# Kernel tuning notes

Hardware: AMD Instinct MI355X
Metric: run time of the kernel (lower is better)

The kernel has to match this reference:

```python
import jax, jax.numpy as jnp
import numpy as np

N, D, NH, NC, B, NL = 400, 256, 4, 2, 64, 2
HD = D // NH


def _ln(x, g, b, eps=1e-5):
    mu = x.mean(-1, keepdims=True)
    var = ((x - mu) ** 2).mean(-1, keepdims=True)
    return (x - mu) * jax.lax.rsqrt(var + eps) * g + b


def _mha(q, kv, wqkv, bqkv, wo, bo):
    # torch nn.MultiheadAttention (batch_first), eval mode
    wq, wk, wv = jnp.split(wqkv, 3, axis=0)
    bq, bk, bv = jnp.split(bqkv, 3, axis=0)
    Bsz, Sq, _ = q.shape
    Sk = kv.shape[1]
    qh = (q @ wq.T + bq).reshape(Bsz, Sq, NH, HD).transpose(0, 2, 1, 3)
    kh = (kv @ wk.T + bk).reshape(Bsz, Sk, NH, HD).transpose(0, 2, 1, 3)
    vh = (kv @ wv.T + bv).reshape(Bsz, Sk, NH, HD).transpose(0, 2, 1, 3)
    scores = jnp.einsum('bhqd,bhkd->bhqk', qh, kh) / jnp.sqrt(jnp.float32(HD))
    attn = jax.nn.softmax(scores, axis=-1)
    o = jnp.einsum('bhqk,bhkd->bhqd', attn, vh)
    o = o.transpose(0, 2, 1, 3).reshape(Bsz, Sq, D)
    return o @ wo.T + bo


def setup_inputs() -> dict:
    key = jax.random.key(0)
    ks = iter(jax.random.split(key, 64))
    w = lambda *s: (jax.random.normal(next(ks), s, dtype=jnp.float32) * 0.02)
    inp = {
        'fc_matrix': jax.random.uniform(next(ks), (B, N, N), dtype=jnp.float32),
        'sc_matrix': jax.random.uniform(next(ks), (B, N, N), dtype=jnp.float32),
        'proj_w': w(D, N), 'proj_b': jnp.zeros((D,), jnp.float32),
        'enc_qkv_w': w(NL, 3 * D, D), 'enc_qkv_b': jnp.zeros((NL, 3 * D), jnp.float32),
        'enc_out_w': w(NL, D, D), 'enc_out_b': jnp.zeros((NL, D), jnp.float32),
        'enc_lin1_w': w(NL, 4 * D, D), 'enc_lin1_b': jnp.zeros((NL, 4 * D), jnp.float32),
        'enc_lin2_w': w(NL, D, 4 * D), 'enc_lin2_b': jnp.zeros((NL, D), jnp.float32),
        'enc_n1_g': jnp.ones((NL, D), jnp.float32), 'enc_n1_b': jnp.zeros((NL, D), jnp.float32),
        'enc_n2_g': jnp.ones((NL, D), jnp.float32), 'enc_n2_b': jnp.zeros((NL, D), jnp.float32),
        'gcn_w1': w(D, N), 'gcn_b1': jnp.zeros((D,), jnp.float32),
        'gcn_w2': w(D, D), 'gcn_b2': jnp.zeros((D,), jnp.float32),
        'ca1_qkv_w': w(3 * D, D), 'ca1_qkv_b': jnp.zeros((3 * D,), jnp.float32),
        'ca1_out_w': w(D, D), 'ca1_out_b': jnp.zeros((D,), jnp.float32),
        'ca1_n_g': jnp.ones((D,), jnp.float32), 'ca1_n_b': jnp.zeros((D,), jnp.float32),
        'ca2_qkv_w': w(3 * D, D), 'ca2_qkv_b': jnp.zeros((3 * D,), jnp.float32),
        'ca2_out_w': w(D, D), 'ca2_out_b': jnp.zeros((D,), jnp.float32),
        'ca2_n_g': jnp.ones((D,), jnp.float32), 'ca2_n_b': jnp.zeros((D,), jnp.float32),
        'cls_w1': w(128, N * D), 'cls_b1': jnp.zeros((128,), jnp.float32),
        'cls_w2': w(NC, 128), 'cls_b2': jnp.zeros((NC,), jnp.float32),
    }
    return inp


def reference(fc_matrix, sc_matrix, proj_w, proj_b,
              enc_qkv_w, enc_qkv_b, enc_out_w, enc_out_b,
              enc_lin1_w, enc_lin1_b, enc_lin2_w, enc_lin2_b,
              enc_n1_g, enc_n1_b, enc_n2_g, enc_n2_b,
              gcn_w1, gcn_b1, gcn_w2, gcn_b2,
              ca1_qkv_w, ca1_qkv_b, ca1_out_w, ca1_out_b, ca1_n_g, ca1_n_b,
              ca2_qkv_w, ca2_qkv_b, ca2_out_w, ca2_out_b, ca2_n_g, ca2_n_b,
              cls_w1, cls_b1, cls_w2, cls_b2):
    # ---- FC branch: input proj + 2 post-norm transformer encoder layers ----
    h = fc_matrix @ proj_w.T + proj_b  # [B,N,D]
    for l in range(NL):
        a = _mha(h, h, enc_qkv_w[l], enc_qkv_b[l], enc_out_w[l], enc_out_b[l])
        h = _ln(h + a, enc_n1_g[l], enc_n1_b[l])
        ff = jax.nn.relu(h @ enc_lin1_w[l].T + enc_lin1_b[l]) @ enc_lin2_w[l].T + enc_lin2_b[l]
        h = _ln(h + ff, enc_n2_g[l], enc_n2_b[l])
    Z_F = h

    # ---- SC branch: dense-equivalent of per-sample nonzero()+GCNConv ----
    # all entries of sc are nonzero -> edge set == dense adjacency (self-loops present,
    # so add_remaining_self_loops is a no-op). deg = in-degree (column sums of weights).
    deg = sc_matrix.sum(axis=-2)  # [B,N]
    dinv = jnp.where(deg > 0, jax.lax.rsqrt(deg), 0.0)
    An = dinv[:, :, None] * sc_matrix * dinv[:, None, :]  # An[b,i,j] = dinv_i * w_ij * dinv_j
    h1 = jnp.einsum('bij,bid->bjd', An, sc_matrix @ gcn_w1.T) + gcn_b1  # aggregate src->dst
    h1 = jax.nn.relu(h1)
    Z_S = jnp.einsum('bij,bid->bjd', An, h1 @ gcn_w2.T) + gcn_b2  # [B,N,D]

    # ---- Cross attention (eval: dropout = identity) ----
    Z_F_cross = _ln(Z_F + _mha(Z_F, Z_S, ca1_qkv_w, ca1_qkv_b, ca1_out_w, ca1_out_b), ca1_n_g, ca1_n_b)
    Z_S_cross = _ln(Z_S + _mha(Z_S, Z_F, ca2_qkv_w, ca2_qkv_b, ca2_out_w, ca2_out_b), ca2_n_g, ca2_n_b)

    Z_joint = (Z_F_cross + Z_S_cross) * 0.5
    flat = Z_joint.reshape(Z_joint.shape[0], -1)  # [B, N*D]
    logits = jax.nn.relu(flat @ cls_w1.T + cls_b1) @ cls_w2.T + cls_b2
    return logits
```

## Files before the change

kernel.cpp:

```cpp
#include <hip/hip_runtime.h>
#include <math.h>

#define NB   64
#define NN   400
#define DD   256
#define NHH  4
#define HDD  64
#define MR   25600

typedef __attribute__((ext_vector_type(8))) short bf16x8;
typedef __attribute__((ext_vector_type(4))) float f32x4;

__device__ __forceinline__ short f2bf(float x) {
    union { float f; unsigned u; } v; v.f = x;
    return (short)((v.u + 0x7FFFu + ((v.u >> 16) & 1u)) >> 16);
}
__device__ __forceinline__ float bf2f(short s) {
    union { unsigned u; float f; } v; v.u = ((unsigned)(unsigned short)s) << 16;
    return v.f;
}
__device__ __forceinline__ void gl_lds16(const void* g, void* l) {
    __builtin_amdgcn_global_load_lds(
        (const __attribute__((address_space(1))) unsigned*)g,
        (__attribute__((address_space(3))) unsigned*)l, 16, 0, 0);
}
__device__ __forceinline__ void wait_vmcnt(int n) {
    switch (n) {
    case 0: asm volatile("s_waitcnt vmcnt(0)" ::: "memory"); break;
    case 1: asm volatile("s_waitcnt vmcnt(1)" ::: "memory"); break;
    case 2: asm volatile("s_waitcnt vmcnt(2)" ::: "memory"); break;
    case 3: asm volatile("s_waitcnt vmcnt(3)" ::: "memory"); break;
    case 4: asm volatile("s_waitcnt vmcnt(4)" ::: "memory"); break;
    default: asm volatile("s_waitcnt vmcnt(5)" ::: "memory"); break;
    }
}
__device__ __forceinline__ void barrier_raw() {
    __builtin_amdgcn_sched_barrier(0);
    __builtin_amdgcn_s_barrier();
    __builtin_amdgcn_sched_barrier(0);
}


__global__ __launch_bounds__(256) void gemm_p8(
    const short* __restrict__ A, int arows, long long sA,
    const short* __restrict__ B, int brows, long long sB,
    const float* __restrict__ bias,
    short* __restrict__ C, int crows, int crz, long long sCe,
    int M, int N, int Npad, int K, int relu)
{
    __shared__ short lds[24576];
    const int tid = threadIdx.x;
    const int z = blockIdx.z;
    const int m0 = blockIdx.x * 128, n0 = blockIdx.y * 128;
    const short* Ab = A + (size_t)z * sA;
    const short* Bb = B + (size_t)z * sB;

    const int w = tid >> 6, lane = tid & 63;
    const int quad = lane >> 4, l15 = lane & 15;
    const int wm = w & 1, wn = w >> 1;

    f32x4 acc[4][4] = {};

    const int KT = K >> 5;

    auto STAGE = [&](int buf, int kt) {
        const int gp0 = kt << 2;
        short* Al = lds + buf * 8192;
        short* Bl = Al + 4096;
#pragma unroll
        for (int i = 0; i < 4; ++i) {
            int c = i * 4 + w;
            int p = (c >> 1) & 3, hh = c & 1;
            if (c < 8)
                gl_lds16(Ab + ((size_t)(gp0 + p) * arows + m0 + hh * 64 + lane) * 8,
                         &Al[(p * 128 + hh * 64) * 8]);
            else
                gl_lds16(Bb + ((size_t)(gp0 + p) * brows + n0 + hh * 64 + lane) * 8,
                         &Bl[(p * 128 + hh * 64) * 8]);
        }
    };

    STAGE(0, 0);
    STAGE(1, 1);
    for (int kt = 0; kt < KT; ++kt) {
        wait_vmcnt(kt + 1 < KT ? 4 : 0);
        barrier_raw();
        if (kt + 2 < KT) STAGE((kt + 2) % 3, kt + 2);
        const short* Al = lds + (kt % 3) * 8192;
        const short* Bl = Al + 4096;
        bf16x8 af[4], bfr[4];
#pragma unroll
        for (int mi = 0; mi < 4; ++mi)
            af[mi] = *reinterpret_cast<const bf16x8*>(
                &Al[(quad * 128 + wm * 64 + mi * 16 + l15) * 8]);
#pragma unroll
        for (int ni = 0; ni < 4; ++ni)
            bfr[ni] = *reinterpret_cast<const bf16x8*>(
                &Bl[(quad * 128 + wn * 64 + ni * 16 + l15) * 8]);
#pragma unroll
        for (int mi = 0; mi < 4; ++mi)
#pragma unroll
            for (int ni = 0; ni < 4; ++ni)
                acc[mi][ni] = __builtin_amdgcn_mfma_f32_16x16x32_bf16(af[mi], bfr[ni], acc[mi][ni], 0, 0, 0);
    }
    __syncthreads();

#pragma unroll
    for (int mi = 0; mi < 4; ++mi) {
#pragma unroll
        for (int r = 0; r < 4; ++r) {
            int row = wm * 64 + mi * 16 + quad * 4 + r;
#pragma unroll
            for (int ni = 0; ni < 4; ++ni) {
                int col = wn * 64 + ni * 16 + l15;
                int gcol = n0 + col;
                float v = 0.0f;
                if (gcol < N) {
                    v = acc[mi][ni][r];
                    if (bias) v += bias[gcol];
                    if (relu) v = fmaxf(v, 0.0f);
                }
                lds[row * 136 + col] = f2bf(v);
            }
        }
    }
    __syncthreads();
    short* Cbz = C + (size_t)z * sCe;
    const long long zr = (long long)z * crz;
#pragma unroll
    for (int t = 0; t < 8; ++t) {
        int c = t * 256 + tid;
        int row = c & 127, p16 = c >> 7;
        int grow = m0 + row;
        int gcol0 = n0 + p16 * 8;
        if (grow < M && gcol0 < Npad) {
            bf16x8 v = *reinterpret_cast<const bf16x8*>(&lds[row * 136 + p16 * 8]);
            *reinterpret_cast<bf16x8*>(
                &Cbz[((size_t)(gcol0 >> 3) * crows + zr + grow) * 8]) = v;
        }
    }
}

__global__ __launch_bounds__(256) void gemm_ln(
    const short* __restrict__ A,
    const short* __restrict__ B, int brows,
    const float* __restrict__ bias,
    const short* __restrict__ resid,
    const float* __restrict__ g, const float* __restrict__ bb,
    short* __restrict__ out, int K)
{
    __shared__ short lds[30720];
    __shared__ float gs[256], bs[256], bi_s[256];
    __shared__ float red[2][4][64];
    const int tid = threadIdx.x;
    const int m0 = blockIdx.x * 64;
    const int w = tid >> 6, lane = tid & 63;
    const int quad = lane >> 4, l15 = lane & 15;
    gs[tid] = g[tid]; bs[tid] = bb[tid]; bi_s[tid] = bias[tid];

    f32x4 acc[16] = {};
    const int KT = K >> 5;

    auto STAGE = [&](int buf, int kt) {
        const int gp0 = kt << 2;
        short* Al = lds + buf * 10240;
        short* Bl = Al + 2048;
#pragma unroll
        for (int i = 0; i < 5; ++i) {
            int c = i * 4 + w;
            if (c < 4) {
                gl_lds16(A + ((size_t)(gp0 + c) * MR + m0 + lane) * 8, &Al[(c * 64) * 8]);
            } else {
                int cb = c - 4, p = cb >> 2, cq = cb & 3;
                gl_lds16(B + ((size_t)(gp0 + p) * brows + cq * 64 + lane) * 8,
                         &Bl[(p * 256 + cq * 64) * 8]);
            }
        }
    };

    STAGE(0, 0);
    STAGE(1, 1);
    for (int kt = 0; kt < KT; ++kt) {
        wait_vmcnt(kt + 1 < KT ? 5 : 0);
        barrier_raw();
        if (kt + 2 < KT) STAGE((kt + 2) % 3, kt + 2);
        const short* Al = lds + (kt % 3) * 10240;
        const short* Bl = Al + 2048;
        bf16x8 af = *reinterpret_cast<const bf16x8*>(
            &Al[(quad * 64 + w * 16 + l15) * 8]);
#pragma unroll
        for (int ni = 0; ni < 16; ++ni) {
            bf16x8 bfr = *reinterpret_cast<const bf16x8*>(
                &Bl[(quad * 256 + ni * 16 + l15) * 8]);
            acc[ni] = __builtin_amdgcn_mfma_f32_16x16x32_bf16(af, bfr, acc[ni], 0, 0, 0);
        }
    }
    __syncthreads();

    short* rowt = lds;
#pragma unroll
    for (int ni = 0; ni < 16; ++ni) {
        int col = ni * 16 + l15;
        int part = col >> 6, idx = col & 63;
#pragma unroll
        for (int r = 0; r < 4; ++r) {
            int row = w * 16 + quad * 4 + r;
            rowt[row * 264 + part * 66 + idx] = f2bf(acc[ni][r] + bi_s[col]);
        }
    }
    __syncthreads();

    const int row = tid >> 2, part = tid & 3;
    const int grow = m0 + row;
    float vv[8][8];
    float sum = 0.0f, sq = 0.0f;
#pragma unroll
    for (int i = 0; i < 8; ++i) {
        int plane = part * 8 + i;
        bf16x8 rv = *reinterpret_cast<const bf16x8*>(resid + ((size_t)plane * MR + grow) * 8);
        bf16x8 tv = *reinterpret_cast<const bf16x8*>(&rowt[row * 264 + part * 66 + i * 8]);
#pragma unroll
        for (int e = 0; e < 8; ++e) {
            float v = bf2f(tv[e]) + bf2f(rv[e]);
            vv[i][e] = v; sum += v; sq += v * v;
        }
    }
    red[0][part][row] = sum; red[1][part][row] = sq;
    __syncthreads();
    sum = red[0][0][row] + red[0][1][row] + red[0][2][row] + red[0][3][row];
    sq  = red[1][0][row] + red[1][1][row] + red[1][2][row] + red[1][3][row];
    float mu = sum * (1.0f / 256.0f);
    float var = sq * (1.0f / 256.0f) - mu * mu;
    float rstd = 1.0f / sqrtf(fmaxf(var, 0.0f) + 1e-5f);
#pragma unroll
    for (int i = 0; i < 8; ++i) {
        int plane = part * 8 + i;
        bf16x8 o;
#pragma unroll
        for (int e = 0; e < 8; ++e)
            o[e] = f2bf((vv[i][e] - mu) * rstd * gs[plane * 8 + e] + bs[plane * 8 + e]);
        *reinterpret_cast<bf16x8*>(out + ((size_t)plane * MR + grow) * 8) = o;
    }
}

__global__ __launch_bounds__(256) void vtrans(
    const short* __restrict__ qkv, short* __restrict__ vT)
{
    __shared__ short tile[64][66];
    const int id = blockIdx.x;
    const int xcd = id & 7, rem = id >> 3;
    const int bh_hi = rem / 7, c = rem - bh_hi * 7;
    const int bh_i = bh_hi * 8 + xcd;
    const int h = bh_i & 3, b = bh_i >> 2;
    const int tid = threadIdx.x;
    const size_t bh = (size_t)bh_i;
    for (int t = tid; t < 512; t += 256) {
        int pp = t >> 6, l = t & 63;
        int j = c * 64 + l;
        bf16x8 v;
        if (j < NN)
            v = *reinterpret_cast<const bf16x8*>(
                qkv + (((size_t)(64 + 8 * h + pp)) * MR + (size_t)b * NN + j) * 8);
        else { for (int e = 0; e < 8; ++e) v[e] = 0; }
#pragma unroll
        for (int e = 0; e < 8; ++e) tile[l][pp * 8 + e] = v[e];
    }
    __syncthreads();
    for (int t = tid; t < 512; t += 256) {
        int kq = t >> 6, d = t & 63;
        int kp = c * 8 + kq;
        bf16x8 o;
#pragma unroll
        for (int e = 0; e < 8; ++e) o[e] = tile[kq * 8 + e][d];
        *reinterpret_cast<bf16x8*>(vT + ((bh * 56 + kp) * 64 + d) * 8) = o;
    }
}

__global__ __launch_bounds__(256, 3) void attn_p8(
    const short* __restrict__ qkv, const short* __restrict__ vT,
    short* __restrict__ Out)
{
    __shared__ short PS[26624];
    const int id = blockIdx.x;
    const int xcd = id & 7, rem = id >> 3;
    const int bh_hi = rem / 7, qt = rem - bh_hi * 7;
    const int bh_i = bh_hi * 8 + xcd;
    const int h = bh_i & 3, b = bh_i >> 2;
    const int tid = threadIdx.x;
    const int w = tid >> 6, lane = tid & 63;
    const int quad = lane >> 4, l15 = lane & 15;
    const size_t rowb = (size_t)b * NN;

    for (int j = w; j < 8; j += 4)
        gl_lds16(qkv + (((size_t)(8 * h + j)) * MR + rowb + qt * 64 + lane) * 8, &PS[j * 512]);
    __syncthreads();

    bf16x8 aq0 = *reinterpret_cast<const bf16x8*>(&PS[(quad * 64 + w * 16 + l15) * 8]);
    bf16x8 aq1 = *reinterpret_cast<const bf16x8*>(&PS[((4 + quad) * 64 + w * 16 + l15) * 8]);

    const short* Kb0 = qkv + ((size_t)(32 + 8 * h + quad) * MR + rowb + l15) * 8;
    const short* Kb1 = qkv + ((size_t)(36 + 8 * h + quad) * MR + rowb + l15) * 8;

    f32x4 sacc[25];
#pragma unroll
    for (int nt = 0; nt < 25; ++nt) { sacc[nt][0] = 0; sacc[nt][1] = 0; sacc[nt][2] = 0; sacc[nt][3] = 0; }
#pragma unroll
    for (int nt = 0; nt < 25; ++nt) {
        bf16x8 b0 = *reinterpret_cast<const bf16x8*>(Kb0 + nt * 128);
        bf16x8 b1 = *reinterpret_cast<const bf16x8*>(Kb1 + nt * 128);
        sacc[nt] = __builtin_amdgcn_mfma_f32_16x16x32_bf16(aq0, b0, sacc[nt], 0, 0, 0);
        sacc[nt] = __builtin_amdgcn_mfma_f32_16x16x32_bf16(aq1, b1, sacc[nt], 0, 0, 0);
    }

    float mx[4] = {-3e38f, -3e38f, -3e38f, -3e38f}, sm[4] = {0, 0, 0, 0};
#pragma unroll
    for (int nt = 0; nt < 25; ++nt)
#pragma unroll
        for (int r = 0; r < 4; ++r) mx[r] = fmaxf(mx[r], sacc[nt][r]);
#pragma unroll
    for (int r = 0; r < 4; ++r) {
        mx[r] = fmaxf(mx[r], __shfl_xor(mx[r], 1));
        mx[r] = fmaxf(mx[r], __shfl_xor(mx[r], 2));
        mx[r] = fmaxf(mx[r], __shfl_xor(mx[r], 4));
        mx[r] = fmaxf(mx[r], __shfl_xor(mx[r], 8));
    }
#pragma unroll
    for (int nt = 0; nt < 25; ++nt)
#pragma unroll
        for (int r = 0; r < 4; ++r) {
            float e = __expf((sacc[nt][r] - mx[r]) * 0.125f);
            sacc[nt][r] = e;
            sm[r] += e;
        }
#pragma unroll
    for (int r = 0; r < 4; ++r) {
        sm[r] += __shfl_xor(sm[r], 1);
        sm[r] += __shfl_xor(sm[r], 2);
        sm[r] += __shfl_xor(sm[r], 4);
        sm[r] += __shfl_xor(sm[r], 8);
    }
    __syncthreads();

#pragma unroll
    for (int nt = 0; nt < 25; ++nt)
#pragma unroll
        for (int r = 0; r < 4; ++r) {
            int colk = nt * 16 + l15;
            PS[((colk >> 3) * 64 + w * 16 + quad * 4 + r) * 8 + (colk & 7)] = f2bf(sacc[nt][r]);
        }
    for (int idx = tid; idx < 1024; idx += 256) PS[25600 + idx] = 0;

    f32x4 oacc[4];
#pragma unroll
    for (int dt = 0; dt < 4; ++dt) { oacc[dt][0] = 0; oacc[dt][1] = 0; oacc[dt][2] = 0; oacc[dt][3] = 0; }
    __syncthreads();

    const short* Vb = vT + (((size_t)bh_i * 56 + quad) * 64 + l15) * 8;
#pragma unroll
    for (int kt = 0; kt < 13; ++kt) {
        bf16x8 pa = *reinterpret_cast<const bf16x8*>(
            &PS[((kt * 4 + quad) * 64 + w * 16 + l15) * 8]);
#pragma unroll
        for (int dt = 0; dt < 4; ++dt) {
            bf16x8 vb = *reinterpret_cast<const bf16x8*>(Vb + kt * 2048 + dt * 128);
            oacc[dt] = __builtin_amdgcn_mfma_f32_16x16x32_bf16(pa, vb, oacc[dt], 0, 0, 0);
        }
    }
#pragma unroll
    for (int r = 0; r < 4; ++r) {
        int row = qt * 64 + w * 16 + quad * 4 + r;
        if (row >= NN) continue;
        float inv = 1.0f / sm[r];
#pragma unroll
        for (int dt = 0; dt < 4; ++dt) {
            int col = dt * 16 + l15;
            Out[(((size_t)(8 * h + (col >> 3))) * MR + rowb + row) * 8 + (col & 7)] =
                f2bf(oacc[dt][r] * inv);
        }
    }
}

__global__ void conv_p8(const float* __restrict__ src, short* __restrict__ dst,
                        int R, int K, int Kp, int PR)
{
    const int G = Kp >> 3;
    int idx = blockIdx.x * 256 + threadIdx.x;
    if (idx >= R * G) return;
    int r = idx / G, g = idx - r * G;
    int k0 = g << 3;
    bf16x8 o;
    if (k0 + 8 <= K) {
        const float4 v0 = *reinterpret_cast<const float4*>(src + (size_t)r * K + k0);
        const float4 v1 = *reinterpret_cast<const float4*>(src + (size_t)r * K + k0 + 4);
        o[0] = f2bf(v0.x); o[1] = f2bf(v0.y); o[2] = f2bf(v0.z); o[3] = f2bf(v0.w);
        o[4] = f2bf(v1.x); o[5] = f2bf(v1.y); o[6] = f2bf(v1.z); o[7] = f2bf(v1.w);
    } else {
#pragma unroll
        for (int e = 0; e < 8; ++e) {
            int k = k0 + e;
            o[e] = (k < K) ? f2bf(src[(size_t)r * K + k]) : (short)0;
        }
    }
    *reinterpret_cast<bf16x8*>(dst + ((size_t)g * PR + r) * 8) = o;
}

__global__ __launch_bounds__(256) void w1_p8(
    const float* __restrict__ W1, short* __restrict__ Wp)
{
    __shared__ float tile[128][129];
    const int k0 = blockIdx.x * 128;
    const int tid = threadIdx.x;
    for (int t = 0; t < 16; ++t) {
        int idx = t * 256 + tid;
        int r = idx >> 5, k4 = idx & 31;
        float4 v = *(const float4*)(W1 + (size_t)r * 102400 + k0 + k4 * 4);
        tile[r][k4 * 4 + 0] = v.x; tile[r][k4 * 4 + 1] = v.y;
        tile[r][k4 * 4 + 2] = v.z; tile[r][k4 * 4 + 3] = v.w;
    }
    __syncthreads();
    for (int t = 0; t < 8; ++t) {
        int idx = t * 256 + tid;
        int pidx = idx >> 7, r = idx & 127;
        bf16x8 o;
#pragma unroll
        for (int e = 0; e < 8; ++e) o[e] = f2bf(tile[r][pidx * 8 + e]);
        *reinterpret_cast<bf16x8*>(Wp + (((size_t)(k0 >> 3) + pidx) * 128 + r) * 8) = o;
    }
}

__global__ void colsum_dinv(const float* __restrict__ sc, float* __restrict__ dinv)
{
    int b = blockIdx.y;
    int j = blockIdx.x * 256 + threadIdx.x;
    if (j >= NN) return;
    const float* p = sc + (size_t)b * NN * NN + j;
    float s = 0.0f;
    for (int i = 0; i < NN; ++i) s += p[(size_t)i * NN];
    dinv[b * NN + j] = (s > 0.0f) ? 1.0f / sqrtf(s) : 0.0f;
}

__global__ __launch_bounds__(256) void sc_prep(
    const float* __restrict__ sc, const float* __restrict__ dinv,
    short* __restrict__ scb, short* __restrict__ anT)
{
    __shared__ float tile[64][65];
    const int b = blockIdx.z;
    const int i0 = blockIdx.y * 64, j0 = blockIdx.x * 64;
    const int tid = threadIdx.x;
    const float* sb = sc + (size_t)b * NN * NN;
    short* scbb = scb + (size_t)b * 56 * 512 * 8;
    short* anTb = anT + (size_t)b * 56 * 512 * 8;
    for (int e = tid; e < 4096; e += 256) {
        int r = e >> 6, c = e & 63;
        int i = i0 + r, j = j0 + c;
        tile[r][c] = (i < NN && j < NN) ? sb[(size_t)i * NN + j] : 0.0f;
    }
    __syncthreads();
    for (int e = tid; e < 4096; e += 256) {
        int r = e >> 6, c = e & 63;
        int i = i0 + r, j = j0 + c;
        scbb[((size_t)(j >> 3) * 512 + i) * 8 + (j & 7)] = f2bf(tile[r][c]);
        float v = 0.0f;
        if (i < NN && j < NN) v = tile[r][c] * dinv[b * NN + i] * dinv[b * NN + j];
        anTb[((size_t)(i >> 3) * 512 + j) * 8 + (i & 7)] = f2bf(v);
    }
}

__global__ __launch_bounds__(256) void cls_gemm(
    const short* __restrict__ C1, const short* __restrict__ C2,
    const short* __restrict__ Wp, float* __restrict__ partial)
{
    __shared__ short Al[32 * 64 * 8];
    __shared__ short Wl[8 * 128 * 8];
    const int j = blockIdx.x;
    const int tid = threadIdx.x;
    const int w = tid >> 6, lane = tid & 63;
    const int quad = lane >> 4, l15 = lane & 15;

    for (int s = 0; s < 8; ++s) {
        int idx = s * 256 + tid;
        int p = idx >> 6, b = idx & 63;
        size_t ad = ((size_t)p * MR + (size_t)b * NN + j) * 8;
        bf16x8 a = *reinterpret_cast<const bf16x8*>(C1 + ad);
        bf16x8 c = *reinterpret_cast<const bf16x8*>(C2 + ad);
        bf16x8 o;
#pragma unroll
        for (int e = 0; e < 8; ++e) o[e] = f2bf(0.5f * (bf2f(a[e]) + bf2f(c[e])));
        *reinterpret_cast<bf16x8*>(&Al[(p * 64 + b) * 8]) = o;
    }

    f32x4 acc[4][2] = {};
    const size_t wp0 = (size_t)j * 32;
    for (int s = 0; s < 4; ++s) {
#pragma unroll
        for (int pp = 0; pp < 2; ++pp) {
            int p = w + pp * 4;
            gl_lds16(Wp + ((wp0 + s * 8 + p) * 128 + lane) * 8,      &Wl[(p * 128) * 8]);
            gl_lds16(Wp + ((wp0 + s * 8 + p) * 128 + 64 + lane) * 8, &Wl[(p * 128 + 64) * 8]);
        }
        __syncthreads();
#pragma unroll
        for (int kb = 0; kb < 2; ++kb) {
            bf16x8 af[4], bfr[2];
#pragma unroll
            for (int mi = 0; mi < 4; ++mi)
                af[mi] = *reinterpret_cast<const bf16x8*>(
                    &Al[((s * 8 + kb * 4 + quad) * 64 + mi * 16 + l15) * 8]);
#pragma unroll
            for (int ni = 0; ni < 2; ++ni)
                bfr[ni] = *reinterpret_cast<const bf16x8*>(
                    &Wl[((kb * 4 + quad) * 128 + w * 32 + ni * 16 + l15) * 8]);
#pragma unroll
            for (int mi = 0; mi < 4; ++mi)
#pragma unroll
                for (int ni = 0; ni < 2; ++ni)
                    acc[mi][ni] = __builtin_amdgcn_mfma_f32_16x16x32_bf16(af[mi], bfr[ni], acc[mi][ni], 0, 0, 0);
        }
        __syncthreads();
    }
    float* pj = partial + (size_t)j * 8192;
#pragma unroll
    for (int mi = 0; mi < 4; ++mi)
#pragma unroll
        for (int r = 0; r < 4; ++r) {
            int row = mi * 16 + quad * 4 + r;
#pragma unroll
            for (int ni = 0; ni < 2; ++ni)
                pj[row * 128 + w * 32 + ni * 16 + l15] = acc[mi][ni][r];
        }
}

__global__ void cls_reduce(const float* __restrict__ partial, float* __restrict__ clsh)
{
    int o = blockIdx.x * 256 + threadIdx.x;
    float s = 0.0f;
    for (int kb = 0; kb < 400; ++kb) s += partial[(size_t)kb * 8192 + o];
    clsh[o] = s;
}

__global__ void logits_final(
    const float* __restrict__ clsh, const float* __restrict__ b1,
    const float* __restrict__ w2, const float* __restrict__ b2,
    float* __restrict__ out)
{
    __shared__ float t[128];
    int b = blockIdx.x;
    int tid = threadIdx.x;
    t[tid] = fmaxf(clsh[b * 128 + tid] + b1[tid], 0.0f);
    __syncthreads();
    if (tid < 2) {
        float s = b2[tid];
        for (int o = 0; o < 128; ++o) s += t[o] * w2[tid * 128 + o];
        out[b * 2 + tid] = s;
    }
}

extern "C" void kernel_launch(void* const* d_in, const int* in_sizes, int n_in,
                              void* d_out, int out_size, void* d_ws, size_t ws_size,
                              hipStream_t stream)
{
    const float* fc        = (const float*)d_in[0];
    const float* sc        = (const float*)d_in[1];
    const float* proj_w    = (const float*)d_in[2];
    const float* proj_b    = (const float*)d_in[3];
    const float* enc_qkv_w = (const float*)d_in[4];
    const float* enc_qkv_b = (const float*)d_in[5];
    const float* enc_out_w = (const float*)d_in[6];
    const float* enc_out_b = (const float*)d_in[7];
    const float* enc_l1_w  = (const float*)d_in[8];
    const float* enc_l1_b  = (const float*)d_in[9];
    const float* enc_l2_w  = (const float*)d_in[10];
    const float* enc_l2_b  = (const float*)d_in[11];
    const float* enc_n1_g  = (const float*)d_in[12];
    const float* enc_n1_b  = (const float*)d_in[13];
    const float* enc_n2_g  = (const float*)d_in[14];
    const float* enc_n2_b  = (const float*)d_in[15];
    const float* gcn_w1    = (const float*)d_in[16];
    const float* gcn_b1    = (const float*)d_in[17];
    const float* gcn_w2    = (const float*)d_in[18];
    const float* gcn_b2    = (const float*)d_in[19];
    const float* ca1_qkv_w = (const float*)d_in[20];
    const float* ca1_qkv_b = (const float*)d_in[21];
    const float* ca1_out_w = (const float*)d_in[22];
    const float* ca1_out_b = (const float*)d_in[23];
    const float* ca1_n_g   = (const float*)d_in[24];
    const float* ca1_n_b   = (const float*)d_in[25];
    const float* ca2_qkv_w = (const float*)d_in[26];
    const float* ca2_qkv_b = (const float*)d_in[27];
    const float* ca2_out_w = (const float*)d_in[28];
    const float* ca2_out_b = (const float*)d_in[29];
    const float* ca2_n_g   = (const float*)d_in[30];
    const float* ca2_n_b   = (const float*)d_in[31];
    const float* cls_w1    = (const float*)d_in[32];
    const float* cls_b1    = (const float*)d_in[33];
    const float* cls_w2    = (const float*)d_in[34];
    const float* cls_b2    = (const float*)d_in[35];

    char* wsb = (char*)d_ws;
    size_t off = 0;
    auto alloc = [&](size_t bytes) { char* r = wsb + off; off += (bytes + 255) & ~(size_t)255; return r; };
    short* bufBig = (short*)alloc((size_t)MR * 1024 * 2);
    short* fcb    = (short*)alloc((size_t)56 * MR * 8 * 2);
    short* anT    = (short*)alloc((size_t)NB * 56 * 512 * 8 * 2);
    short* bufH   = (short*)alloc((size_t)32 * MR * 8 * 2);
    short* bufA   = (short*)alloc((size_t)32 * MR * 8 * 2);
    short* bufC   = (short*)alloc((size_t)32 * MR * 8 * 2);
    short* bufZS  = (short*)alloc((size_t)32 * MR * 8 * 2);
    short* vT     = (short*)alloc((size_t)NB * NHH * 56 * 64 * 8 * 2);
    short* w1b    = (short*)alloc((size_t)12800 * 128 * 8 * 2);
    short* projwb = (short*)alloc((size_t)56 * 256 * 8 * 2);
    short* qkvwb  = (short*)alloc((size_t)32 * 1536 * 8 * 2);
    short* outwb  = (short*)alloc((size_t)32 * 512 * 8 * 2);
    short* l1wb   = (short*)alloc((size_t)32 * 2048 * 8 * 2);
    short* l2wb   = (short*)alloc((size_t)128 * 512 * 8 * 2);
    short* gw1b   = (short*)alloc((size_t)56 * 256 * 8 * 2);
    short* gw2b   = (short*)alloc((size_t)32 * 256 * 8 * 2);
    short* c1qb   = (short*)alloc((size_t)32 * 768 * 8 * 2);
    short* c1ob   = (short*)alloc((size_t)32 * 256 * 8 * 2);
    short* c2qb   = (short*)alloc((size_t)32 * 768 * 8 * 2);
    short* c2ob   = (short*)alloc((size_t)32 * 256 * 8 * 2);
    float* dinv   = (float*)alloc((size_t)MR * 4);
    float* clsh   = (float*)alloc((size_t)NB * 128 * 4);
    short* scb = bufBig;
    short* XT1 = bufBig + (size_t)64 * 56 * 512 * 8;
    short* h1  = bufBig;
    short* XT2 = XT1;
    float* partial = (float*)fcb;

    dim3 blk(256);
    auto cgrid = [](long long n) { return dim3((unsigned)((n + 255) / 256)); };

    conv_p8<<<cgrid((long long)MR * 56), blk, 0, stream>>>(fc, fcb, MR, 400, 448, MR);
    conv_p8<<<cgrid(256 * 56), blk, 0, stream>>>(proj_w, projwb, 256, 400, 448, 256);
    conv_p8<<<cgrid(1536 * 32), blk, 0, stream>>>(enc_qkv_w, qkvwb, 1536, 256, 256, 1536);
    conv_p8<<<cgrid(512 * 32), blk, 0, stream>>>(enc_out_w, outwb, 512, 256, 256, 512);
    conv_p8<<<cgrid(2048 * 32), blk, 0, stream>>>(enc_l1_w, l1wb, 2048, 256, 256, 2048);
    conv_p8<<<cgrid(512 * 128), blk, 0, stream>>>(enc_l2_w, l2wb, 512, 1024, 1024, 512);
    conv_p8<<<cgrid(256 * 56), blk, 0, stream>>>(gcn_w1, gw1b, 256, 400, 448, 256);
    conv_p8<<<cgrid(256 * 32), blk, 0, stream>>>(gcn_w2, gw2b, 256, 256, 256, 256);
    conv_p8<<<cgrid(768 * 32), blk, 0, stream>>>(ca1_qkv_w, c1qb, 768, 256, 256, 768);
    conv_p8<<<cgrid(256 * 32), blk, 0, stream>>>(ca1_out_w, c1ob, 256, 256, 256, 256);
    conv_p8<<<cgrid(768 * 32), blk, 0, stream>>>(ca2_qkv_w, c2qb, 768, 256, 256, 768);
    conv_p8<<<cgrid(256 * 32), blk, 0, stream>>>(ca2_out_w, c2ob, 256, 256, 256, 256);
    w1_p8<<<800, blk, 0, stream>>>(cls_w1, w1b);

    gemm_p8<<<dim3(200, 2, 1), blk, 0, stream>>>(
        fcb, MR, 0, projwb, 256, 0, proj_b, bufH, MR, 0, 0, MR, 256, 256, 448, 0);
    for (int l = 0; l < 2; ++l) {
        gemm_p8<<<dim3(200, 6, 1), blk, 0, stream>>>(
            bufH, MR, 0, qkvwb + (size_t)l * 768 * 8, 1536, 0, enc_qkv_b + l * 768,
            bufBig, MR, 0, 0, MR, 768, 768, 256, 0);
        vtrans<<<dim3(1792), blk, 0, stream>>>(bufBig, vT);
        attn_p8<<<dim3(1792), blk, 0, stream>>>(bufBig, vT, bufA);
        gemm_ln<<<400, blk, 0, stream>>>(
            bufA, outwb + (size_t)l * 256 * 8, 512, enc_out_b + l * 256,
            bufH, enc_n1_g + l * DD, enc_n1_b + l * DD, bufH, 256);
        gemm_p8<<<dim3(200, 8, 1), blk, 0, stream>>>(
            bufH, MR, 0, l1wb + (size_t)l * 1024 * 8, 2048, 0, enc_l1_b + l * 1024,
            bufBig, MR, 0, 0, MR, 1024, 1024, 256, 1);
        gemm_ln<<<400, blk, 0, stream>>>(
            bufBig, l2wb + (size_t)l * 256 * 8, 512, enc_l2_b + l * 256,
            bufH, enc_n2_g + l * DD, enc_n2_b + l * DD, bufH, 1024);
    }

    colsum_dinv<<<dim3(2, NB), blk, 0, stream>>>(sc, dinv);
    sc_prep<<<dim3(7, 7, NB), blk, 0, stream>>>(sc, dinv, scb, anT);
    gemm_p8<<<dim3(2, 4, NB), blk, 0, stream>>>(
        gw1b, 256, 0, scb, 512, 56LL * 512 * 8, nullptr,
        XT1, 256, 0, 56LL * 256 * 8, 256, 400, 448, 448, 0);
    gemm_p8<<<dim3(4, 2, NB), blk, 0, stream>>>(
        anT, 512, 56LL * 512 * 8, XT1, 256, 56LL * 256 * 8, gcn_b1,
        h1, 512, 0, 32LL * 512 * 8, 400, 256, 256, 448, 1);
    gemm_p8<<<dim3(2, 4, NB), blk, 0, stream>>>(
        gw2b, 256, 0, h1, 512, 32LL * 512 * 8, nullptr,
        XT2, 256, 0, 56LL * 256 * 8, 256, 400, 448, 256, 0);
    gemm_p8<<<dim3(4, 2, NB), blk, 0, stream>>>(
        anT, 512, 56LL * 512 * 8, XT2, 256, 56LL * 256 * 8, gcn_b2,
        bufZS, MR, 400, 0, 400, 256, 256, 448, 0);

    gemm_p8<<<dim3(200, 2, 1), blk, 0, stream>>>(
        bufH, MR, 0, c1qb, 768, 0, ca1_qkv_b, bufBig, MR, 0, 0, MR, 256, 256, 256, 0);
    gemm_p8<<<dim3(200, 4, 1), blk, 0, stream>>>(
        bufZS, MR, 0, c1qb + 256 * 8, 768, 0, ca1_qkv_b + 256,
        bufBig + (size_t)32 * MR * 8, MR, 0, 0, MR, 512, 512, 256, 0);
    vtrans<<<dim3(1792), blk, 0, stream>>>(bufBig, vT);
    attn_p8<<<dim3(1792), blk, 0, stream>>>(bufBig, vT, bufA);
    gemm_ln<<<400, blk, 0, stream>>>(
        bufA, c1ob, 256, ca1_out_b, bufH, ca1_n_g, ca1_n_b, bufC, 256);

    gemm_p8<<<dim3(200, 2, 1), blk, 0, stream>>>(
        bufZS, MR, 0, c2qb, 768, 0, ca2_qkv_b, bufBig, MR, 0, 0, MR, 256, 256, 256, 0);
    gemm_p8<<<dim3(200, 4, 1), blk, 0, stream>>>(
        bufH, MR, 0, c2qb + 256 * 8, 768, 0, ca2_qkv_b + 256,
        bufBig + (size_t)32 * MR * 8, MR, 0, 0, MR, 512, 512, 256, 0);
    vtrans<<<dim3(1792), blk, 0, stream>>>(bufBig, vT);
    attn_p8<<<dim3(1792), blk, 0, stream>>>(bufBig, vT, bufA);
    gemm_ln<<<400, blk, 0, stream>>>(
        bufA, c2ob, 256, ca2_out_b, bufZS, ca2_n_g, ca2_n_b, bufZS, 256);

    cls_gemm<<<400, blk, 0, stream>>>(bufC, bufZS, w1b, partial);
    cls_reduce<<<32, blk, 0, stream>>>(partial, clsh);
    logits_final<<<NB, 128, 0, stream>>>(clsh, cls_b1, cls_w2, cls_b2, (float*)d_out);
}
```

Baseline: 974.2 us.

## Load GEMM MFMA fragments directly from global memory into double-buffered registers

Replaces the triple-buffered global-to-LDS staging in the bf16 GEMM main loop with direct per-wave global loads into registers. Two register sets alternate so the next k-tile loads while MFMAs run on the current one. This removes the per-iteration barriers and LDS reads. LDS shrinks to just the epilogue buffer. In exchange, A and B fragments are fetched redundantly by the two waves that share them, which leans on cache bandwidth. The loop steps two k-tiles at a time and assumes an even tile count.

```diff
diff --git a/kernel.cpp b/kernel.cpp
--- a/kernel.cpp
+++ b/kernel.cpp
@@ -48,7 +48,7 @@
     short* __restrict__ C, int crows, int crz, long long sCe,
     int M, int N, int Npad, int K, int relu)
 {
-    __shared__ short lds[24576];
+    __shared__ short lds[17408];
     const int tid = threadIdx.x;
     const int z = blockIdx.z;
     const int m0 = blockIdx.x * 128, n0 = blockIdx.y * 128;
@@ -59,51 +59,37 @@
     const int quad = lane >> 4, l15 = lane & 15;
     const int wm = w & 1, wn = w >> 1;
 
+    const short* Abase = Ab + (((size_t)quad * arows) + m0 + wm * 64 + l15) * 8;
+    const short* Bbase = Bb + (((size_t)quad * brows) + n0 + wn * 64 + l15) * 8;
+    const size_t stepA = (size_t)4 * arows * 8;
+    const size_t stepB = (size_t)4 * brows * 8;
+
     f32x4 acc[4][4] = {};
-
     const int KT = K >> 5;
 
-    auto STAGE = [&](int buf, int kt) {
-        const int gp0 = kt << 2;
-        short* Al = lds + buf * 8192;
-        short* Bl = Al + 4096;
-#pragma unroll
-        for (int i = 0; i < 4; ++i) {
-            int c = i * 4 + w;
-            int p = (c >> 1) & 3, hh = c & 1;
-            if (c < 8)
-                gl_lds16(Ab + ((size_t)(gp0 + p) * arows + m0 + hh * 64 + lane) * 8,
-                         &Al[(p * 128 + hh * 64) * 8]);
-            else
-                gl_lds16(Bb + ((size_t)(gp0 + p) * brows + n0 + hh * 64 + lane) * 8,
-                         &Bl[(p * 128 + hh * 64) * 8]);
-        }
-    };
-
-    STAGE(0, 0);
-    STAGE(1, 1);
-    for (int kt = 0; kt < KT; ++kt) {
-        wait_vmcnt(kt + 1 < KT ? 4 : 0);
-        barrier_raw();
-        if (kt + 2 < KT) STAGE((kt + 2) % 3, kt + 2);
-        const short* Al = lds + (kt % 3) * 8192;
-        const short* Bl = Al + 4096;
-        bf16x8 af[4], bfr[4];
-#pragma unroll
-        for (int mi = 0; mi < 4; ++mi)
-            af[mi] = *reinterpret_cast<const bf16x8*>(
-                &Al[(quad * 128 + wm * 64 + mi * 16 + l15) * 8]);
-#pragma unroll
-        for (int ni = 0; ni < 4; ++ni)
-            bfr[ni] = *reinterpret_cast<const bf16x8*>(
-                &Bl[(quad * 128 + wn * 64 + ni * 16 + l15) * 8]);
-#pragma unroll
-        for (int mi = 0; mi < 4; ++mi)
-#pragma unroll
-            for (int ni = 0; ni < 4; ++ni)
-                acc[mi][ni] = __builtin_amdgcn_mfma_f32_16x16x32_bf16(af[mi], bfr[ni], acc[mi][ni], 0, 0, 0);
-    }
-    __syncthreads();
+    bf16x8 a0[4], b0[4], a1[4], b1[4];
+
+#define LOADA(d, kt) { const short* _p = Abase + (size_t)(kt) * stepA; \
+    _Pragma("unroll") for (int mi = 0; mi < 4; ++mi) \
+        d[mi] = *reinterpret_cast<const bf16x8*>(_p + mi * 128); }
+#define LOADB(d, kt) { const short* _p = Bbase + (size_t)(kt) * stepB; \
+    _Pragma("unroll") for (int ni = 0; ni < 4; ++ni) \
+        d[ni] = *reinterpret_cast<const bf16x8*>(_p + ni * 128); }
+#define MFMA16(af, bfr) { \
+    _Pragma("unroll") for (int mi = 0; mi < 4; ++mi) \
+    _Pragma("unroll") for (int ni = 0; ni < 4; ++ni) \
+        acc[mi][ni] = __builtin_amdgcn_mfma_f32_16x16x32_bf16(af[mi], bfr[ni], acc[mi][ni], 0, 0, 0); }
+
+    LOADA(a0, 0); LOADB(b0, 0);
+    for (int kt = 0; kt < KT; kt += 2) {
+        LOADA(a1, kt + 1); LOADB(b1, kt + 1);
+        MFMA16(a0, b0);
+        if (kt + 2 < KT) { LOADA(a0, kt + 2); LOADB(b0, kt + 2); }
+        MFMA16(a1, b1);
+    }
+#undef LOADA
+#undef LOADB
+#undef MFMA16
 
 #pragma unroll
     for (int mi = 0; mi < 4; ++mi) {
```

Measured after the change: 1.020 ms. +4.7%, slower.
